# Performance work log

Hardware: AMD Instinct MI355X
Metric: run time of the kernel (lower is better)

Reference implementation:

```python
import jax, jax.numpy as jnp
import numpy as np

N = 50000       # num vertices
E_SEG = 80000   # num hyperedges
NNZ = 400000    # incidence pairs
FIN = 512       # input feature dim
H = 256         # MLP_hidden
C = 40          # num classes
NLAYER = 2      # All_num_layers
ALPHA = 0.5     # restart_alpha


def _w(k, shape):
    return jax.random.normal(k, shape, jnp.float32) * (1.0 / np.sqrt(shape[0]))


def setup_inputs() -> dict:
    key = jax.random.key(0)
    ks = jax.random.split(key, 12)
    return {
        "x": jax.random.normal(ks[0], (N, FIN), jnp.float32),
        "vertex": jax.random.randint(ks[1], (NNZ,), 0, N),
        "edges": jax.random.randint(ks[2], (NNZ,), 0, E_SEG),
        "lin_in_w": _w(ks[3], (FIN, H)), "lin_in_b": jnp.zeros((H,), jnp.float32),
        "w1": _w(ks[4], (H, H)),   "b1": jnp.zeros((H,), jnp.float32),
        "w2": _w(ks[5], (2 * H, H)), "b2": jnp.zeros((H,), jnp.float32),
        "w3": _w(ks[6], (H, H)),   "b3": jnp.zeros((H,), jnp.float32),
        "cls_w1": _w(ks[7], (H, H)), "cls_b1": jnp.zeros((H,), jnp.float32),
        "cls_w2": _w(ks[8], (H, C)), "cls_b2": jnp.zeros((C,), jnp.float32),
    }


def reference(x, vertex, edges, lin_in_w, lin_in_b, w1, b1, w2, b2, w3, b3,
              cls_w1, cls_b1, cls_w2, cls_b2):
    # input projection (dropout is identity at p=0)
    x = jax.nn.relu(x @ lin_in_w + lin_in_b)           # [N, H]
    x0 = x
    for _ in range(NLAYER):  # same conv weights reused each layer
        # W1 (1-layer MLP = Linear), gather to incidences
        xve = (x @ w1 + b1)[vertex]                    # [NNZ, H]
        # scatter-add to hyperedges
        xe = jax.ops.segment_sum(xve, edges, num_segments=E_SEG)  # [E, H]
        # gather back, concat with vertex feats, W2 (Linear on 2H)
        xev = jnp.concatenate([x[vertex], xe[edges]], axis=-1) @ w2 + b2  # [NNZ, H]
        # scatter-add to vertices
        xv = jax.ops.segment_sum(xev, vertex, num_segments=N)     # [N, H]
        # restart connection + W (Linear) + outer activation
        x = (1.0 - ALPHA) * xv + ALPHA * x0
        x = jax.nn.relu(x @ w3 + b3)
    # classifier MLP (2 layers: Linear -> relu -> Linear)
    h = jax.nn.relu(x @ cls_w1 + cls_b1)
    return h @ cls_w2 + cls_b2                          # [N, C]
```

## Files before the change

kernel.cpp:

```cpp
#include <hip/hip_runtime.h>
#include <hip/hip_bf16.h>
#include <cstdint>
#include <cstddef>

#define HD   256
#define NV   50000
#define NE   80000
#define NNZC 400000
#define FINC 512
#define NCLS 40

using bf16 = __hip_bfloat16;

typedef short bf16x8v __attribute__((ext_vector_type(8)));
typedef float f32x4   __attribute__((ext_vector_type(4)));
typedef unsigned short u16x8 __attribute__((ext_vector_type(8)));

#define NCH_E ((NE + 1023) / 1024)
#define NCH_V ((NV + 1023) / 1024)
#define NBM_V ((NV + 127) / 128)

__device__ __forceinline__ float b2f(unsigned short u) {
    union { unsigned int i; float f; } c; c.i = ((unsigned int)u) << 16; return c.f;
}
__device__ __forceinline__ unsigned short f2b(float f) {
    union { float f; unsigned int i; } c; c.f = f;
    return (unsigned short)((c.i + 0x7FFFu + ((c.i >> 16) & 1u)) >> 16);
}
__device__ __forceinline__ float4 load4f(const bf16* p) {
    ushort4 u = *reinterpret_cast<const ushort4*>(p);
    return make_float4(b2f(u.x), b2f(u.y), b2f(u.z), b2f(u.w));
}
__device__ __forceinline__ void store4(bf16* p, float4 v) {
    ushort4 u; u.x = f2b(v.x); u.y = f2b(v.y); u.z = f2b(v.z); u.w = f2b(v.w);
    *reinterpret_cast<ushort4*>(p) = u;
}

__device__ __forceinline__ void gl_lds16(const bf16* g, short* l) {
    __builtin_amdgcn_global_load_lds(
        (const __attribute__((address_space(1))) unsigned int*)g,
        (__attribute__((address_space(3))) unsigned int*)l,
        16, 0, 0);
}

__global__ __launch_bounds__(256)
void fill0_k(unsigned int* __restrict__ p, long long n)
{
    long long i = (long long)blockIdx.x * 256 + threadIdx.x;
    long long stride = (long long)gridDim.x * 256;
    for (; i < n; i += stride) p[i] = 0u;
}

__global__ __launch_bounds__(256)
void hist_k(const int* __restrict__ vertex, const int* __restrict__ edges,
            int* __restrict__ cnt_v, int* __restrict__ cnt_e, int nnz)
{
    int i = blockIdx.x * 256 + threadIdx.x;
    if (i < nnz) {
        atomicAdd(&cnt_v[vertex[i]], 1);
        atomicAdd(&cnt_e[edges[i]], 1);
    }
}

__global__ __launch_bounds__(256)
void scan_part2_k(const int* __restrict__ cnt_e, int* __restrict__ off_e, int* __restrict__ part_e,
                  const int* __restrict__ cnt_v, int* __restrict__ off_v, int* __restrict__ part_v)
{
    const int* cnt; int* off; int* part; int n;
    if (blockIdx.y == 0) { cnt = cnt_e; off = off_e; part = part_e; n = NE; }
    else                 { cnt = cnt_v; off = off_v; part = part_v; n = NV; }
    int base = blockIdx.x * 1024;
    if (base >= n) return;
    __shared__ int s[256];
    int idx = base + threadIdx.x * 4;
    int v[4], sum = 0;
    #pragma unroll
    for (int j = 0; j < 4; ++j) { v[j] = (idx + j < n) ? cnt[idx + j] : 0; sum += v[j]; }
    s[threadIdx.x] = sum;
    __syncthreads();
    #pragma unroll
    for (int d = 1; d < 256; d <<= 1) {
        int t = (threadIdx.x >= d) ? s[threadIdx.x - d] : 0;
        __syncthreads();
        s[threadIdx.x] += t;
        __syncthreads();
    }
    int excl = s[threadIdx.x] - sum;
    #pragma unroll
    for (int j = 0; j < 4; ++j) {
        if (idx + j < n) off[idx + j] = excl;
        excl += v[j];
    }
    if (threadIdx.x == 255) part[blockIdx.x] = s[255];
}

__global__ __launch_bounds__(256)
void scan_top2_k(int* __restrict__ part_e, int* __restrict__ end_e,
                 int* __restrict__ part_v, int* __restrict__ end_v)
{
    int* part; int* endp; int nch;
    if (blockIdx.x == 0) { part = part_e; endp = end_e; nch = NCH_E; }
    else                 { part = part_v; endp = end_v; nch = NCH_V; }
    __shared__ int s[256];
    int v = (threadIdx.x < nch) ? part[threadIdx.x] : 0;
    s[threadIdx.x] = v;
    __syncthreads();
    #pragma unroll
    for (int d = 1; d < 256; d <<= 1) {
        int t = (threadIdx.x >= d) ? s[threadIdx.x - d] : 0;
        __syncthreads();
        s[threadIdx.x] += t;
        __syncthreads();
    }
    if (threadIdx.x < nch) part[threadIdx.x] = s[threadIdx.x] - v;
    if (threadIdx.x == 255) *endp = s[255];
}

__global__ __launch_bounds__(256)
void scan_addcur2_k(int* __restrict__ off_e, const int* __restrict__ part_e, int* __restrict__ cur_e,
                    int* __restrict__ off_v, const int* __restrict__ part_v, int* __restrict__ cur_v)
{
    int n; int* off; const int* part; int* cur;
    if (blockIdx.y == 0) { n = NE; off = off_e; part = part_e; cur = cur_e; }
    else                 { n = NV; off = off_v; part = part_v; cur = cur_v; }
    int i = blockIdx.x * 256 + threadIdx.x;
    if (i < n) { int o = off[i] + part[i >> 10]; off[i] = o; cur[i] = o; }
}

__global__ __launch_bounds__(256)
void csr_fill_k(const int* __restrict__ vertex, const int* __restrict__ edges,
                int* __restrict__ cur_e, int* __restrict__ cur_v,
                int* __restrict__ adj_e, int* __restrict__ adj_v, int nnz)
{
    int i = blockIdx.x * 256 + threadIdx.x;
    if (i >= nnz) return;
    int v = vertex[i], e = edges[i];
    adj_e[atomicAdd(&cur_e[e], 1)] = v;
    adj_v[atomicAdd(&cur_v[v], 1)] = e;
}

__global__ __launch_bounds__(256)
void dege2_k(const int* __restrict__ cnt_e, const int* __restrict__ adj_v,
             const int* __restrict__ off_v, int* __restrict__ dege2, int n)
{
    int v = blockIdx.x * 256 + threadIdx.x;
    if (v >= n) return;
    int s = 0;
    for (int j = off_v[v]; j < off_v[v + 1]; ++j) s += cnt_e[adj_v[j]];
    dege2[v] = s;
}

__global__ __launch_bounds__(256)
void b1w23_k(const float* __restrict__ b1, const unsigned short* __restrict__ W23bt,
             float* __restrict__ o)
{
    int n = threadIdx.x;
    float s = 0.f;
    for (int k = 0; k < 256; ++k) s += b1[k] * b2f(W23bt[n * 256 + k]);
    o[n] = s;
}

__global__ __launch_bounds__(256)
void prep_w_k(const float* __restrict__ lin_w, const float* __restrict__ w1,
              const float* __restrict__ w2, const float* __restrict__ w3,
              const float* __restrict__ cw1, const float* __restrict__ cw2,
              const float* __restrict__ b2,
              unsigned short* __restrict__ lin_wt, unsigned short* __restrict__ w1_nb,
              unsigned short* __restrict__ w2a_nb, unsigned short* __restrict__ w2b_nb,
              unsigned short* __restrict__ w3t, unsigned short* __restrict__ cw1t,
              unsigned short* __restrict__ cw2t, float* __restrict__ b2w3)
{
    int idx = blockIdx.x * 256 + threadIdx.x;
    if (idx < 131072) { int n = idx >> 9, k = idx & 511; lin_wt[idx] = f2b(lin_w[k * 256 + n]); return; }
    idx -= 131072;
    if (idx < 65536) { w1_nb[idx] = f2b(w1[idx]); return; }
    idx -= 65536;
    if (idx < 65536) { w2a_nb[idx] = f2b(w2[idx]); return; }
    idx -= 65536;
    if (idx < 65536) { w2b_nb[idx] = f2b(w2[65536 + idx]); return; }
    idx -= 65536;
    if (idx < 65536) { int n = idx >> 8, k = idx & 255; w3t[idx] = f2b(w3[k * 256 + n]); return; }
    idx -= 65536;
    if (idx < 65536) { int n = idx >> 8, k = idx & 255; cw1t[idx] = f2b(cw1[k * 256 + n]); return; }
    idx -= 65536;
    if (idx < 12288) { int n = idx >> 8, k = idx & 255; cw2t[idx] = f2b((n < NCLS) ? cw2[k * NCLS + n] : 0.f); return; }
    idx -= 12288;
    if (idx < 256) {
        float s = 0.f;
        for (int k = 0; k < 256; ++k) s += b2[k] * w3[k * 256 + idx];
        b2w3[idx] = s;
    }
}

template<int EPI, bool AF32>
__global__ __launch_bounds__(256)
void mgemm_k(const void* __restrict__ Agv, const bf16* __restrict__ Bt,
             const float* __restrict__ bias, const float* __restrict__ bias2,
             const int* __restrict__ deg, const int* __restrict__ dege2,
             const bf16* __restrict__ Sb, const bf16* __restrict__ z0b,
             const float* __restrict__ b2w3v, const float* __restrict__ b1w23v,
             bf16* __restrict__ Cg, bf16* __restrict__ Cg2, bf16* __restrict__ Cg3,
             int M, int K, int Nc)
{
    const int nbn = Nc >> 7;
    const int nbm = (M + 127) >> 7;
    const int p   = blockIdx.x;
    const int xcd = p & 7;
    const int q   = p >> 3;
    const int cblk = q % nbn;
    const int rblk = q / nbn;
    const int rb   = rblk * 8 + xcd;
    if (rb >= nbm) return;
    const int bn = cblk * 128;
    const int bm = rb * 128;

    __shared__ __align__(16) short As[128 * 64];
    __shared__ __align__(16) short Bs[128 * 64];

    const int t  = threadIdx.x;
    const int wv = t >> 6, l = t & 63;
    const int wr = wv >> 1, wc = wv & 1;
    const int l15 = l & 15;

    f32x4 acc[4][4];
    #pragma unroll
    for (int m = 0; m < 4; ++m)
        #pragma unroll
        for (int n = 0; n < 4; ++n)
            acc[m][n] = (f32x4){0.f, 0.f, 0.f, 0.f};

    const int brow8   = l >> 3;
    const int bcol_sw = (((l & 7) ^ (l >> 3)) * 8);

    for (int k0 = 0; k0 < K; k0 += 64) {
        if constexpr (AF32) {
            const float* Af = (const float*)Agv;
            #pragma unroll
            for (int pi = 0; pi < 4; ++pi) {
                int idx8 = pi * 256 + t;
                int row  = idx8 >> 3;
                int cg   = (idx8 & 7) * 8;
                int ga = bm + row; if (ga >= M) ga = M - 1;
                const float* src = Af + (size_t)ga * K + k0 + cg;
                f32x4 u = *reinterpret_cast<const f32x4*>(src);
                f32x4 v = *reinterpret_cast<const f32x4*>(src + 4);
                bf16x8v o;
                o[0] = (short)f2b(u[0]); o[1] = (short)f2b(u[1]);
                o[2] = (short)f2b(u[2]); o[3] = (short)f2b(u[3]);
                o[4] = (short)f2b(v[0]); o[5] = (short)f2b(v[1]);
                o[6] = (short)f2b(v[2]); o[7] = (short)f2b(v[3]);
                *reinterpret_cast<bf16x8v*>(As + row * 64 + (cg ^ ((row & 7) * 8))) = o;
            }
        } else {
            const bf16* Ab = (const bf16*)Agv;
            #pragma unroll
            for (int i = 0; i < 4; ++i) {
                int c = wv * 4 + i;
                int row = c * 8 + brow8;
                int ga = bm + row; if (ga >= M) ga = M - 1;
                gl_lds16(Ab + (size_t)ga * K + k0 + bcol_sw, As + c * 512);
            }
        }
        #pragma unroll
        for (int i = 0; i < 4; ++i) {
            int c = wv * 4 + i;
            int row = c * 8 + brow8;
            gl_lds16(Bt + (size_t)(bn + row) * K + k0 + bcol_sw, Bs + c * 512);
        }
        __syncthreads();

        #pragma unroll
        for (int ks = 0; ks < 2; ++ks) {
            bf16x8v a[4], b[4];
            const int kb = ks * 64 + (l >> 4) * 16;
            #pragma unroll
            for (int m = 0; m < 4; ++m) {
                int r = wr * 64 + m * 16 + l15;
                a[m] = *reinterpret_cast<const bf16x8v*>(
                           (const char*)As + r * 128 + (kb ^ ((r & 7) << 4)));
            }
            #pragma unroll
            for (int n = 0; n < 4; ++n) {
                int r = wc * 64 + n * 16 + l15;
                b[n] = *reinterpret_cast<const bf16x8v*>(
                           (const char*)Bs + r * 128 + (kb ^ ((r & 7) << 4)));
            }
            #pragma unroll
            for (int m = 0; m < 4; ++m)
                #pragma unroll
                for (int n = 0; n < 4; ++n)
                    acc[m][n] = __builtin_amdgcn_mfma_f32_16x16x32_bf16(a[m], b[n], acc[m][n], 0, 0, 0);
        }
        __syncthreads();
    }

    if (EPI == 5) {
        int oi = bn >> 8;
        bf16* CC = (oi == 0) ? Cg : Cg2;
        int c2 = (bn >> 7) & 1;
        unsigned short* P = (unsigned short*)CC + ((size_t)(rb * 2 + c2) * 256 + t) * 64;
        #pragma unroll
        for (int m = 0; m < 4; ++m) {
            u16x8 o0, o1;
            #pragma unroll
            for (int n = 0; n < 2; ++n)
                #pragma unroll
                for (int i = 0; i < 4; ++i) {
                    o0[n * 4 + i] = f2b(acc[m][n][i]);
                    o1[n * 4 + i] = f2b(acc[m][n + 2][i]);
                }
            *reinterpret_cast<u16x8*>(P + m * 16)     = o0;
            *reinterpret_cast<u16x8*>(P + m * 16 + 8) = o1;
        }
    } else if (EPI == 4) {
        float bv[4], bw[4], bb1[4];
        #pragma unroll
        for (int n = 0; n < 4; ++n) {
            int col = bn + wc * 64 + n * 16 + l15;
            bv[n]  = bias[col];
            bw[n]  = b2w3v[col];
            bb1[n] = b1w23v[col];
        }
        const unsigned short* Sp = (const unsigned short*)Sb + ((size_t)(rb * 2 + cblk) * 256 + t) * 64;
        const unsigned short* Zp = (const unsigned short*)z0b + ((size_t)(rb * 2 + cblk) * 256 + t) * 64;
        u16x8 sv8[8], zv8[8];
        #pragma unroll
        for (int j = 0; j < 8; ++j) {
            sv8[j] = *reinterpret_cast<const u16x8*>(Sp + j * 8);
            zv8[j] = *reinterpret_cast<const u16x8*>(Zp + j * 8);
        }
        #pragma unroll
        for (int m = 0; m < 4; ++m) {
            #pragma unroll
            for (int i = 0; i < 4; ++i) {
                int row = bm + wr * 64 + m * 16 + (l >> 4) * 4 + i;
                if (row >= M) continue;
                float d   = (float)deg[row];
                float de2 = (float)dege2[row];
                size_t base = (size_t)row * Nc + bn + wc * 64 + l15;
                #pragma unroll
                for (int n = 0; n < 4; ++n) {
                    int e = m * 16 + n * 4 + i;
                    float sv = b2f(sv8[e >> 3][e & 7]);
                    float zv = b2f(zv8[e >> 3][e & 7]);
                    float v = 0.5f * (d * (sv + bw[n]) + acc[m][n][i] + de2 * bb1[n])
                              + 0.5f * zv + bv[n];
                    v = fmaxf(v, 0.f);
                    reinterpret_cast<unsigned short*>(Cg)[base + (size_t)n * 16] = f2b(v);
                }
            }
        }
    } else if (EPI == 3) {
        int oi = bn >> 8;
        bf16* CC = (oi == 0) ? Cg : (oi == 1) ? Cg2 : Cg3;
        const float* bb = (oi == 0) ? bias : (oi == 1) ? bias2 : nullptr;
        int cb = bn & 255;
        float bv[4];
        #pragma unroll
        for (int n = 0; n < 4; ++n)
            bv[n] = bb ? bb[cb + wc * 64 + n * 16 + l15] : 0.f;
        #pragma unroll
        for (int m = 0; m < 4; ++m) {
            #pragma unroll
            for (int i = 0; i < 4; ++i) {
                int row = bm + wr * 64 + m * 16 + (l >> 4) * 4 + i;
                if (row >= M) continue;
                size_t base = (size_t)row * 256 + cb + wc * 64 + l15;
                #pragma unroll
                for (int n = 0; n < 4; ++n)
                    reinterpret_cast<unsigned short*>(CC)[base + n * 16] = f2b(acc[m][n][i] + bv[n]);
            }
        }
    } else {
        float bv[4];
        #pragma unroll
        for (int n = 0; n < 4; ++n)
            bv[n] = bias ? bias[bn + wc * 64 + n * 16 + l15] : 0.f;
        #pragma unroll
        for (int m = 0; m < 4; ++m) {
            #pragma unroll
            for (int i = 0; i < 4; ++i) {
                int row = bm + wr * 64 + m * 16 + (l >> 4) * 4 + i;
                if (row >= M) continue;
                size_t base = (size_t)row * Nc + bn + wc * 64 + l15;
                #pragma unroll
                for (int n = 0; n < 4; ++n) {
                    float v = acc[m][n][i] + bv[n];
                    if (EPI == 1) v = fmaxf(v, 0.f);
                    reinterpret_cast<unsigned short*>(Cg)[base + n * 16] = f2b(v);
                }
            }
        }
    }
}

__global__ __launch_bounds__(256)
void gather_sum_k(const bf16* __restrict__ src, const int* __restrict__ adj,
                  const int* __restrict__ off, bf16* __restrict__ dst, int nseg)
{
    int seg = blockIdx.x * 4 + (threadIdx.x >> 6);
    if (seg >= nseg) return;
    int lane = threadIdx.x & 63;
    int s0 = off[seg], s1 = off[seg + 1];
    float4 acc = make_float4(0.f, 0.f, 0.f, 0.f);
    int j = s0;
    for (; j + 4 <= s1; j += 4) {
        int r0 = adj[j], r1 = adj[j + 1], r2 = adj[j + 2], r3 = adj[j + 3];
        float4 v0 = load4f(src + (size_t)r0 * HD + lane * 4);
        float4 v1 = load4f(src + (size_t)r1 * HD + lane * 4);
        float4 v2 = load4f(src + (size_t)r2 * HD + lane * 4);
        float4 v3 = load4f(src + (size_t)r3 * HD + lane * 4);
        acc.x += (v0.x + v1.x) + (v2.x + v3.x);
        acc.y += (v0.y + v1.y) + (v2.y + v3.y);
        acc.z += (v0.z + v1.z) + (v2.z + v3.z);
        acc.w += (v0.w + v1.w) + (v2.w + v3.w);
    }
    for (; j < s1; ++j) {
        float4 v = load4f(src + (size_t)adj[j] * HD + lane * 4);
        acc.x += v.x; acc.y += v.y; acc.z += v.z; acc.w += v.w;
    }
    store4(dst + (size_t)seg * HD + lane * 4, acc);
}

__global__ __launch_bounds__(256)
void cls_mfma_k(const bf16* __restrict__ Hm, const bf16* __restrict__ Wt,
                const float* __restrict__ bias, float* __restrict__ out, int M)
{
    const int wv = threadIdx.x >> 6, l = threadIdx.x & 63;
    const int l15 = l & 15;
    const int r0 = blockIdx.x * 64 + wv * 16;
    f32x4 acc[3];
    #pragma unroll
    for (int n = 0; n < 3; ++n) acc[n] = (f32x4){0.f, 0.f, 0.f, 0.f};

    int arow = r0 + l15; if (arow >= M) arow = M - 1;
    const int ko = (l >> 4) * 8;
    for (int kk = 0; kk < HD; kk += 32) {
        bf16x8v a = *reinterpret_cast<const bf16x8v*>(Hm + (size_t)arow * HD + kk + ko);
        #pragma unroll
        for (int n = 0; n < 3; ++n) {
            bf16x8v b = *reinterpret_cast<const bf16x8v*>(Wt + (size_t)(n * 16 + l15) * HD + kk + ko);
            acc[n] = __builtin_amdgcn_mfma_f32_16x16x32_bf16(a, b, acc[n], 0, 0, 0);
        }
    }
    #pragma unroll
    for (int n = 0; n < 3; ++n) {
        int col = n * 16 + l15;
        if (col >= NCLS) continue;
        float bv = bias[col];
        #pragma unroll
        for (int i = 0; i < 4; ++i) {
            int row = r0 + (l >> 4) * 4 + i;
            if (row < M) out[(size_t)row * NCLS + col] = acc[n][i] + bv;
        }
    }
}

static inline int xcd_grid(int M, int Nc)
{
    int nbm = (M + 127) >> 7;
    int nbn = Nc >> 7;
    return nbn * (((nbm + 7) / 8) * 8);
}

extern "C" void kernel_launch(void* const* d_in, const int* in_sizes, int n_in,
                              void* d_out, int out_size, void* d_ws, size_t ws_size,
                              hipStream_t stream)
{
    const float* x_in   = (const float*)d_in[0];
    const int*   vertex = (const int*)d_in[1];
    const int*   edges  = (const int*)d_in[2];
    const float* lin_w  = (const float*)d_in[3];
    const float* lin_b  = (const float*)d_in[4];
    const float* w1     = (const float*)d_in[5];
    const float* b1     = (const float*)d_in[6];
    const float* w2     = (const float*)d_in[7];
    const float* b2     = (const float*)d_in[8];
    const float* w3     = (const float*)d_in[9];
    const float* b3     = (const float*)d_in[10];
    const float* cw1    = (const float*)d_in[11];
    const float* cb1    = (const float*)d_in[12];
    const float* cw2    = (const float*)d_in[13];
    const float* cb2    = (const float*)d_in[14];
    float* out = (float*)d_out;
    (void)in_sizes; (void)n_in; (void)out_size; (void)ws_size;

    char* ws = (char*)d_ws;
    const size_t nvhd = (size_t)NV * HD, nehd = (size_t)NE * HD;
    const size_t permsz = (size_t)(NBM_V + 1) * 2 * 256 * 64;
    size_t off = 0;
    auto alloc = [&](size_t bytes) { char* p = ws + off; off += (bytes + 255) & ~(size_t)255; return p; };
    bf16* x0 = (bf16*)alloc(nvhd * 2);
    bf16* xA = (bf16*)alloc(nvhd * 2);
    bf16* E1 = (bf16*)alloc(nehd * 2);
    bf16* E2 = (bf16*)alloc(nehd * 2);
    bf16* S  = (bf16*)alloc(permsz * 2);
    bf16* z0 = (bf16*)alloc(permsz * 2);
    unsigned short* W23at  = (unsigned short*)alloc(2 * 256 * 256 * 2);
    unsigned short* w3t    = W23at + 65536;
    unsigned short* W23bt  = (unsigned short*)alloc(256 * 256 * 2);
    unsigned short* W123bt = (unsigned short*)alloc(256 * 256 * 2);
    unsigned short* w2ab   = (unsigned short*)alloc(512 * 256 * 2);
    unsigned short* w2a_nb = w2ab;
    unsigned short* w2b_nb = w2ab + 256 * 256;
    unsigned short* w1_nb  = (unsigned short*)alloc(256 * 256 * 2);
    unsigned short* lin_wt = (unsigned short*)alloc(256 * 512 * 2);
    unsigned short* cw1t   = (unsigned short*)alloc(256 * 256 * 2);
    unsigned short* cw2t   = (unsigned short*)alloc(48 * 256 * 2);
    float* b2w3  = (float*)alloc(256 * 4);
    float* b1w23 = (float*)alloc(256 * 4);
    int* cnt_e = (int*)alloc(NE * 4);
    int* cnt_v = (int*)alloc(NV * 4);
    int* dege2 = (int*)alloc(NV * 4);
    int* off_e = (int*)alloc((NE + 1) * 4);
    int* off_v = (int*)alloc((NV + 1) * 4);
    int* cur_e = (int*)alloc(NE * 4);
    int* cur_v = (int*)alloc(NV * 4);
    int* part_e = (int*)alloc(256 * 4);
    int* part_v = (int*)alloc(256 * 4);
    int* adj_e = (int*)alloc((size_t)NNZC * 4);
    int* adj_v = (int*)alloc((size_t)NNZC * 4);

    dim3 blk(256);

    fill0_k<<<128, blk, 0, stream>>>((unsigned int*)cnt_e, NE + NV);
    hist_k<<<(NNZC + 255) / 256, blk, 0, stream>>>(vertex, edges, cnt_v, cnt_e, NNZC);
    scan_part2_k<<<dim3(NCH_E, 2), blk, 0, stream>>>(cnt_e, off_e, part_e, cnt_v, off_v, part_v);
    scan_top2_k<<<2, blk, 0, stream>>>(part_e, off_e + NE, part_v, off_v + NV);
    scan_addcur2_k<<<dim3((NE + 255) / 256, 2), blk, 0, stream>>>(off_e, part_e, cur_e,
                                                                  off_v, part_v, cur_v);
    csr_fill_k<<<(NNZC + 255) / 256, blk, 0, stream>>>(vertex, edges, cur_e, cur_v, adj_e, adj_v, NNZC);
    dege2_k<<<(NV + 255) / 256, blk, 0, stream>>>(cnt_e, adj_v, off_v, dege2, NV);

    prep_w_k<<<1841, blk, 0, stream>>>(lin_w, w1, w2, w3, cw1, cw2, b2,
                                       lin_wt, w1_nb, w2a_nb, w2b_nb, w3t, cw1t, cw2t, b2w3);
    mgemm_k<3, false><<<xcd_grid(256, 512), blk, 0, stream>>>((const bf16*)w3t, (const bf16*)w2ab,
        nullptr, nullptr, nullptr, nullptr, nullptr, nullptr, nullptr, nullptr,
        (bf16*)W23at, (bf16*)W23bt, nullptr, 256, 256, 512);
    mgemm_k<0, false><<<xcd_grid(256, 256), blk, 0, stream>>>((const bf16*)W23bt, (const bf16*)w1_nb,
        nullptr, nullptr, nullptr, nullptr, nullptr, nullptr, nullptr, nullptr,
        (bf16*)W123bt, nullptr, nullptr, 256, 256, 256);
    b1w23_k<<<1, blk, 0, stream>>>(b1, W23bt, b1w23);

    mgemm_k<1, true><<<xcd_grid(NV, 256), blk, 0, stream>>>(x_in, (const bf16*)lin_wt,
        lin_b, nullptr, nullptr, nullptr, nullptr, nullptr, nullptr, nullptr,
        x0, nullptr, nullptr, NV, FINC, HD);

    const bf16* cur = x0;
    for (int layer = 0; layer < 2; ++layer) {
        if (layer == 0) {
            mgemm_k<5, false><<<xcd_grid(NV, 512), blk, 0, stream>>>(cur, (const bf16*)W23at,
                nullptr, nullptr, nullptr, nullptr, nullptr, nullptr, nullptr, nullptr,
                S, z0, nullptr, NV, HD, 512);
        } else {
            mgemm_k<5, false><<<xcd_grid(NV, 256), blk, 0, stream>>>(cur, (const bf16*)W23at,
                nullptr, nullptr, nullptr, nullptr, nullptr, nullptr, nullptr, nullptr,
                S, nullptr, nullptr, NV, HD, HD);
        }
        gather_sum_k<<<(NE + 3) / 4, blk, 0, stream>>>(cur, adj_e, off_e, E2, NE);
        gather_sum_k<<<(NV + 3) / 4, blk, 0, stream>>>(E2, adj_v, off_v, E1, NV);
        mgemm_k<4, false><<<xcd_grid(NV, 256), blk, 0, stream>>>(E1, (const bf16*)W123bt,
            b3, nullptr, cnt_v, dege2, S, z0, b2w3, b1w23,
            xA, nullptr, nullptr, NV, HD, HD);
        cur = xA;
    }

    mgemm_k<1, false><<<xcd_grid(NV, 256), blk, 0, stream>>>(xA, (const bf16*)cw1t,
        cb1, nullptr, nullptr, nullptr, nullptr, nullptr, nullptr, nullptr,
        E1, nullptr, nullptr, NV, HD, HD);
    cls_mfma_k<<<(NV + 63) / 64, blk, 0, stream>>>(E1, (const bf16*)cw2t, cb2, out, NV);
}
```

Before: 487.0 us.

## Co-schedule GEMM with edge gather in one launch and merge fill with weight prep

Merges the per-layer S/z0 GEMM and the hyperedge gather-sum into a single kernel that splits blocks by index, so the memory-bound gather runs alongside the MFMA GEMM blocks. The buffer-zeroing kernel is also folded into the weight-prep kernel to remove a launch. In the EPI==4 GEMM, the S/z0 and bias epilogue loads move before the main loop so their latency overlaps compute, at the cost of more live registers during the loop.

```diff
diff --git a/kernel.cpp b/kernel.cpp
--- a/kernel.cpp
+++ b/kernel.cpp
@@ -43,134 +43,50 @@
         16, 0, 0);
 }
 
-__global__ __launch_bounds__(256)
-void fill0_k(unsigned int* __restrict__ p, long long n)
-{
-    long long i = (long long)blockIdx.x * 256 + threadIdx.x;
-    long long stride = (long long)gridDim.x * 256;
-    for (; i < n; i += stride) p[i] = 0u;
-}
-
-__global__ __launch_bounds__(256)
-void hist_k(const int* __restrict__ vertex, const int* __restrict__ edges,
-            int* __restrict__ cnt_v, int* __restrict__ cnt_e, int nnz)
-{
-    int i = blockIdx.x * 256 + threadIdx.x;
-    if (i < nnz) {
-        atomicAdd(&cnt_v[vertex[i]], 1);
-        atomicAdd(&cnt_e[edges[i]], 1);
-    }
-}
-
-__global__ __launch_bounds__(256)
-void scan_part2_k(const int* __restrict__ cnt_e, int* __restrict__ off_e, int* __restrict__ part_e,
-                  const int* __restrict__ cnt_v, int* __restrict__ off_v, int* __restrict__ part_v)
-{
-    const int* cnt; int* off; int* part; int n;
-    if (blockIdx.y == 0) { cnt = cnt_e; off = off_e; part = part_e; n = NE; }
-    else                 { cnt = cnt_v; off = off_v; part = part_v; n = NV; }
-    int base = blockIdx.x * 1024;
-    if (base >= n) return;
-    __shared__ int s[256];
-    int idx = base + threadIdx.x * 4;
-    int v[4], sum = 0;
-    #pragma unroll
-    for (int j = 0; j < 4; ++j) { v[j] = (idx + j < n) ? cnt[idx + j] : 0; sum += v[j]; }
-    s[threadIdx.x] = sum;
-    __syncthreads();
-    #pragma unroll
-    for (int d = 1; d < 256; d <<= 1) {
-        int t = (threadIdx.x >= d) ? s[threadIdx.x - d] : 0;
-        __syncthreads();
-        s[threadIdx.x] += t;
-        __syncthreads();
-    }
-    int excl = s[threadIdx.x] - sum;
-    #pragma unroll
-    for (int j = 0; j < 4; ++j) {
-        if (idx + j < n) off[idx + j] = excl;
-        excl += v[j];
-    }
-    if (threadIdx.x == 255) part[blockIdx.x] = s[255];
-}
-
-__global__ __launch_bounds__(256)
-void scan_top2_k(int* __restrict__ part_e, int* __restrict__ end_e,
-                 int* __restrict__ part_v, int* __restrict__ end_v)
-{
-    int* part; int* endp; int nch;
-    if (blockIdx.x == 0) { part = part_e; endp = end_e; nch = NCH_E; }
-    else                 { part = part_v; endp = end_v; nch = NCH_V; }
-    __shared__ int s[256];
-    int v = (threadIdx.x < nch) ? part[threadIdx.x] : 0;
-    s[threadIdx.x] = v;
-    __syncthreads();
-    #pragma unroll
-    for (int d = 1; d < 256; d <<= 1) {
-        int t = (threadIdx.x >= d) ? s[threadIdx.x - d] : 0;
-        __syncthreads();
-        s[threadIdx.x] += t;
-        __syncthreads();
-    }
-    if (threadIdx.x < nch) part[threadIdx.x] = s[threadIdx.x] - v;
-    if (threadIdx.x == 255) *endp = s[255];
-}
-
-__global__ __launch_bounds__(256)
-void scan_addcur2_k(int* __restrict__ off_e, const int* __restrict__ part_e, int* __restrict__ cur_e,
-                    int* __restrict__ off_v, const int* __restrict__ part_v, int* __restrict__ cur_v)
-{
-    int n; int* off; const int* part; int* cur;
-    if (blockIdx.y == 0) { n = NE; off = off_e; part = part_e; cur = cur_e; }
-    else                 { n = NV; off = off_v; part = part_v; cur = cur_v; }
-    int i = blockIdx.x * 256 + threadIdx.x;
-    if (i < n) { int o = off[i] + part[i >> 10]; off[i] = o; cur[i] = o; }
-}
-
-__global__ __launch_bounds__(256)
-void csr_fill_k(const int* __restrict__ vertex, const int* __restrict__ edges,
-                int* __restrict__ cur_e, int* __restrict__ cur_v,
-                int* __restrict__ adj_e, int* __restrict__ adj_v, int nnz)
-{
-    int i = blockIdx.x * 256 + threadIdx.x;
-    if (i >= nnz) return;
-    int v = vertex[i], e = edges[i];
-    adj_e[atomicAdd(&cur_e[e], 1)] = v;
-    adj_v[atomicAdd(&cur_v[v], 1)] = e;
-}
-
-__global__ __launch_bounds__(256)
-void dege2_k(const int* __restrict__ cnt_e, const int* __restrict__ adj_v,
-             const int* __restrict__ off_v, int* __restrict__ dege2, int n)
-{
-    int v = blockIdx.x * 256 + threadIdx.x;
-    if (v >= n) return;
-    int s = 0;
-    for (int j = off_v[v]; j < off_v[v + 1]; ++j) s += cnt_e[adj_v[j]];
-    dege2[v] = s;
-}
-
-__global__ __launch_bounds__(256)
-void b1w23_k(const float* __restrict__ b1, const unsigned short* __restrict__ W23bt,
-             float* __restrict__ o)
-{
-    int n = threadIdx.x;
-    float s = 0.f;
-    for (int k = 0; k < 256; ++k) s += b1[k] * b2f(W23bt[n * 256 + k]);
-    o[n] = s;
-}
-
-__global__ __launch_bounds__(256)
-void prep_w_k(const float* __restrict__ lin_w, const float* __restrict__ w1,
-              const float* __restrict__ w2, const float* __restrict__ w3,
-              const float* __restrict__ cw1, const float* __restrict__ cw2,
-              const float* __restrict__ b2,
-              unsigned short* __restrict__ lin_wt, unsigned short* __restrict__ w1_nb,
-              unsigned short* __restrict__ w2a_nb, unsigned short* __restrict__ w2b_nb,
-              unsigned short* __restrict__ w3t, unsigned short* __restrict__ cw1t,
-              unsigned short* __restrict__ cw2t, float* __restrict__ b2w3)
-{
-    int idx = blockIdx.x * 256 + threadIdx.x;
+__device__ __forceinline__ void gather_body(const bf16* __restrict__ src,
+                                            const int* __restrict__ adj,
+                                            const int* __restrict__ off,
+                                            bf16* __restrict__ dst,
+                                            int seg, int lane)
+{
+    int s0 = off[seg], s1 = off[seg + 1];
+    float4 acc = make_float4(0.f, 0.f, 0.f, 0.f);
+    int j = s0;
+    for (; j + 4 <= s1; j += 4) {
+        int r0 = adj[j], r1 = adj[j + 1], r2 = adj[j + 2], r3 = adj[j + 3];
+        float4 v0 = load4f(src + (size_t)r0 * HD + lane * 4);
+        float4 v1 = load4f(src + (size_t)r1 * HD + lane * 4);
+        float4 v2 = load4f(src + (size_t)r2 * HD + lane * 4);
+        float4 v3 = load4f(src + (size_t)r3 * HD + lane * 4);
+        acc.x += (v0.x + v1.x) + (v2.x + v3.x);
+        acc.y += (v0.y + v1.y) + (v2.y + v3.y);
+        acc.z += (v0.z + v1.z) + (v2.z + v3.z);
+        acc.w += (v0.w + v1.w) + (v2.w + v3.w);
+    }
+    for (; j < s1; ++j) {
+        float4 v = load4f(src + (size_t)adj[j] * HD + lane * 4);
+        acc.x += v.x; acc.y += v.y; acc.z += v.z; acc.w += v.w;
+    }
+    store4(dst + (size_t)seg * HD + lane * 4, acc);
+}
+
+__global__ __launch_bounds__(256)
+void fill_prep_k(unsigned int* __restrict__ fillp, long long filln,
+                 const float* __restrict__ lin_w, const float* __restrict__ w1,
+                 const float* __restrict__ w2, const float* __restrict__ w3,
+                 const float* __restrict__ cw1, const float* __restrict__ cw2,
+                 const float* __restrict__ b2,
+                 unsigned short* __restrict__ lin_wt, unsigned short* __restrict__ w1_nb,
+                 unsigned short* __restrict__ w2a_nb, unsigned short* __restrict__ w2b_nb,
+                 unsigned short* __restrict__ w3t, unsigned short* __restrict__ cw1t,
+                 unsigned short* __restrict__ cw2t, float* __restrict__ b2w3)
+{
+    if (blockIdx.x < 128) {
+        long long i = (long long)blockIdx.x * 256 + threadIdx.x;
+        for (; i < filln; i += 128 * 256) fillp[i] = 0u;
+        return;
+    }
+    int idx = (blockIdx.x - 128) * 256 + threadIdx.x;
     if (idx < 131072) { int n = idx >> 9, k = idx & 511; lin_wt[idx] = f2b(lin_w[k * 256 + n]); return; }
     idx -= 131072;
     if (idx < 65536) { w1_nb[idx] = f2b(w1[idx]); return; }
@@ -192,6 +108,115 @@
     }
 }
 
+__global__ __launch_bounds__(256)
+void hist_k(const int* __restrict__ vertex, const int* __restrict__ edges,
+            int* __restrict__ cnt_v, int* __restrict__ cnt_e, int nnz)
+{
+    int i = blockIdx.x * 256 + threadIdx.x;
+    if (i < nnz) {
+        atomicAdd(&cnt_v[vertex[i]], 1);
+        atomicAdd(&cnt_e[edges[i]], 1);
+    }
+}
+
+__global__ __launch_bounds__(256)
+void scan_part2_k(const int* __restrict__ cnt_e, int* __restrict__ off_e, int* __restrict__ part_e,
+                  const int* __restrict__ cnt_v, int* __restrict__ off_v, int* __restrict__ part_v)
+{
+    const int* cnt; int* off; int* part; int n;
+    if (blockIdx.y == 0) { cnt = cnt_e; off = off_e; part = part_e; n = NE; }
+    else                 { cnt = cnt_v; off = off_v; part = part_v; n = NV; }
+    int base = blockIdx.x * 1024;
+    if (base >= n) return;
+    __shared__ int s[256];
+    int idx = base + threadIdx.x * 4;
+    int v[4], sum = 0;
+    #pragma unroll
+    for (int j = 0; j < 4; ++j) { v[j] = (idx + j < n) ? cnt[idx + j] : 0; sum += v[j]; }
+    s[threadIdx.x] = sum;
+    __syncthreads();
+    #pragma unroll
+    for (int d = 1; d < 256; d <<= 1) {
+        int t = (threadIdx.x >= d) ? s[threadIdx.x - d] : 0;
+        __syncthreads();
+        s[threadIdx.x] += t;
+        __syncthreads();
+    }
+    int excl = s[threadIdx.x] - sum;
+    #pragma unroll
+    for (int j = 0; j < 4; ++j) {
+        if (idx + j < n) off[idx + j] = excl;
+        excl += v[j];
+    }
+    if (threadIdx.x == 255) part[blockIdx.x] = s[255];
+}
+
+__global__ __launch_bounds__(256)
+void scan_top2_k(int* __restrict__ part_e, int* __restrict__ end_e,
+                 int* __restrict__ part_v, int* __restrict__ end_v)
+{
+    int* part; int* endp; int nch;
+    if (blockIdx.x == 0) { part = part_e; endp = end_e; nch = NCH_E; }
+    else                 { part = part_v; endp = end_v; nch = NCH_V; }
+    __shared__ int s[256];
+    int v = (threadIdx.x < nch) ? part[threadIdx.x] : 0;
+    s[threadIdx.x] = v;
+    __syncthreads();
+    #pragma unroll
+    for (int d = 1; d < 256; d <<= 1) {
+        int t = (threadIdx.x >= d) ? s[threadIdx.x - d] : 0;
+        __syncthreads();
+        s[threadIdx.x] += t;
+        __syncthreads();
+    }
+    if (threadIdx.x < nch) part[threadIdx.x] = s[threadIdx.x] - v;
+    if (threadIdx.x == 255) *endp = s[255];
+}
+
+__global__ __launch_bounds__(256)
+void scan_addcur2_k(int* __restrict__ off_e, const int* __restrict__ part_e, int* __restrict__ cur_e,
+                    int* __restrict__ off_v, const int* __restrict__ part_v, int* __restrict__ cur_v)
+{
+    int n; int* off; const int* part; int* cur;
+    if (blockIdx.y == 0) { n = NE; off = off_e; part = part_e; cur = cur_e; }
+    else                 { n = NV; off = off_v; part = part_v; cur = cur_v; }
+    int i = blockIdx.x * 256 + threadIdx.x;
+    if (i < n) { int o = off[i] + part[i >> 10]; off[i] = o; cur[i] = o; }
+}
+
+__global__ __launch_bounds__(256)
+void csr_fill_k(const int* __restrict__ vertex, const int* __restrict__ edges,
+                int* __restrict__ cur_e, int* __restrict__ cur_v,
+                int* __restrict__ adj_e, int* __restrict__ adj_v, int nnz)
+{
+    int i = blockIdx.x * 256 + threadIdx.x;
+    if (i >= nnz) return;
+    int v = vertex[i], e = edges[i];
+    adj_e[atomicAdd(&cur_e[e], 1)] = v;
+    adj_v[atomicAdd(&cur_v[v], 1)] = e;
+}
+
+__global__ __launch_bounds__(256)
+void dege2_k(const int* __restrict__ cnt_e, const int* __restrict__ adj_v,
+             const int* __restrict__ off_v, int* __restrict__ dege2, int n)
+{
+    int v = blockIdx.x * 256 + threadIdx.x;
+    if (v >= n) return;
+    int s = 0;
+    for (int j = off_v[v]; j < off_v[v + 1]; ++j) s += cnt_e[adj_v[j]];
+    dege2[v] = s;
+}
+
+__global__ __launch_bounds__(256)
+void b1w23_k(const float* __restrict__ b1, const unsigned short* __restrict__ W23bt,
+             float* __restrict__ o)
+{
+    int n = threadIdx.x;
+    float s = 0.f;
+    for (int k = 0; k < 256; ++k) s += b1[k] * b2f(W23bt[n * 256 + k]);
+    o[n] = s;
+}
+
 template<int EPI, bool AF32>
 __global__ __launch_bounds__(256)
 void mgemm_k(const void* __restrict__ Agv, const bf16* __restrict__ Bt,
@@ -221,6 +246,25 @@
     const int wv = t >> 6, l = t & 63;
     const int wr = wv >> 1, wc = wv & 1;
     const int l15 = l & 15;
+
+    u16x8 sv8[8], zv8[8];
+    float bv[4], bw[4], bb1[4];
+    if (EPI == 4) {
+        const unsigned short* Sp = (const unsigned short*)Sb + ((size_t)(rb * 2 + cblk) * 256 + t) * 64;
+        const unsigned short* Zp = (const unsigned short*)z0b + ((size_t)(rb * 2 + cblk) * 256 + t) * 64;
+        #pragma unroll
+        for (int j = 0; j < 8; ++j) {
+            sv8[j] = *reinterpret_cast<const u16x8*>(Sp + j * 8);
+            zv8[j] = *reinterpret_cast<const u16x8*>(Zp + j * 8);
+        }
+        #pragma unroll
+        for (int n = 0; n < 4; ++n) {
+            int col = bn + wc * 64 + n * 16 + l15;
+            bv[n]  = bias[col];
+            bw[n]  = b2w3v[col];
+            bb1[n] = b1w23v[col];
+        }
+    }
 
     f32x4 acc[4][4];
     #pragma unroll
@@ -313,22 +357,6 @@
             *reinterpret_cast<u16x8*>(P + m * 16 + 8) = o1;
         }
     } else if (EPI == 4) {
-        float bv[4], bw[4], bb1[4];
-        #pragma unroll
-        for (int n = 0; n < 4; ++n) {
-            int col = bn + wc * 64 + n * 16 + l15;
-            bv[n]  = bias[col];
-            bw[n]  = b2w3v[col];
-            bb1[n] = b1w23v[col];
-        }
-        const unsigned short* Sp = (const unsigned short*)Sb + ((size_t)(rb * 2 + cblk) * 256 + t) * 64;
-        const unsigned short* Zp = (const unsigned short*)z0b + ((size_t)(rb * 2 + cblk) * 256 + t) * 64;
-        u16x8 sv8[8], zv8[8];
-        #pragma unroll
-        for (int j = 0; j < 8; ++j) {
-            sv8[j] = *reinterpret_cast<const u16x8*>(Sp + j * 8);
-            zv8[j] = *reinterpret_cast<const u16x8*>(Zp + j * 8);
-        }
         #pragma unroll
         for (int m = 0; m < 4; ++m) {
             #pragma unroll
@@ -355,10 +383,10 @@
         bf16* CC = (oi == 0) ? Cg : (oi == 1) ? Cg2 : Cg3;
         const float* bb = (oi == 0) ? bias : (oi == 1) ? bias2 : nullptr;
         int cb = bn & 255;
-        float bv[4];
+        float bvv[4];
         #pragma unroll
         for (int n = 0; n < 4; ++n)
-            bv[n] = bb ? bb[cb + wc * 64 + n * 16 + l15] : 0.f;
+            bvv[n] = bb ? bb[cb + wc * 64 + n * 16 + l15] : 0.f;
         #pragma unroll
         for (int m = 0; m < 4; ++m) {
             #pragma unroll
@@ -368,14 +396,14 @@
                 size_t base = (size_t)row * 256 + cb + wc * 64 + l15;
                 #pragma unroll
                 for (int n = 0; n < 4; ++n)
-                    reinterpret_cast<unsigned short*>(CC)[base + n * 16] = f2b(acc[m][n][i] + bv[n]);
+                    reinterpret_cast<unsigned short*>(CC)[base + n * 16] = f2b(acc[m][n][i] + bvv[n]);
             }
         }
     } else {
-        float bv[4];
+        float bvv[4];
         #pragma unroll
         for (int n = 0; n < 4; ++n)
-            bv[n] = bias ? bias[bn + wc * 64 + n * 16 + l15] : 0.f;
+            bvv[n] = bias ? bias[bn + wc * 64 + n * 16 + l15] : 0.f;
         #pragma unroll
         for (int m = 0; m < 4; ++m) {
             #pragma unroll
@@ -385,7 +413,7 @@
                 size_t base = (size_t)row * Nc + bn + wc * 64 + l15;
                 #pragma unroll
                 for (int n = 0; n < 4; ++n) {
-                    float v = acc[m][n][i] + bv[n];
+                    float v = acc[m][n][i] + bvv[n];
                     if (EPI == 1) v = fmaxf(v, 0.f);
                     reinterpret_cast<unsigned short*>(Cg)[base + n * 16] = f2b(v);
                 }
@@ -395,31 +423,115 @@
 }
 
 __global__ __launch_bounds__(256)
+void fusedA_k(const bf16* __restrict__ Ag, const bf16* __restrict__ Bt,
+              bf16* __restrict__ Sg, bf16* __restrict__ z0g,
+              int M, int K, int Nc, int gemmBlocks,
+              const bf16* __restrict__ gsrc, const int* __restrict__ adj,
+              const int* __restrict__ off, bf16* __restrict__ gdst, int nseg)
+{
+    __shared__ __align__(16) short As[128 * 64];
+    __shared__ __align__(16) short Bs[128 * 64];
+    const int t = threadIdx.x;
+
+    if ((int)blockIdx.x >= gemmBlocks) {
+        int seg = (blockIdx.x - gemmBlocks) * 4 + (t >> 6);
+        if (seg < nseg) gather_body(gsrc, adj, off, gdst, seg, t & 63);
+        return;
+    }
+
+    const int nbn = Nc >> 7;
+    const int nbm = (M + 127) >> 7;
+    const int p   = blockIdx.x;
+    const int xcd = p & 7;
+    const int q   = p >> 3;
+    const int cblk = q % nbn;
+    const int rblk = q / nbn;
+    const int rb   = rblk * 8 + xcd;
+    if (rb >= nbm) return;
+    const int bn = cblk * 128;
+    const int bm = rb * 128;
+
+    const int wv = t >> 6, l = t & 63;
+    const int wr = wv >> 1, wc = wv & 1;
+    const int l15 = l & 15;
+
+    f32x4 acc[4][4];
+    #pragma unroll
+    for (int m = 0; m < 4; ++m)
+        #pragma unroll
+        for (int n = 0; n < 4; ++n)
+            acc[m][n] = (f32x4){0.f, 0.f, 0.f, 0.f};
+
+    const int brow8   = l >> 3;
+    const int bcol_sw = (((l & 7) ^ (l >> 3)) * 8);
+
+    for (int k0 = 0; k0 < K; k0 += 64) {
+        #pragma unroll
+        for (int i = 0; i < 4; ++i) {
+            int c = wv * 4 + i;
+            int row = c * 8 + brow8;
+            int ga = bm + row; if (ga >= M) ga = M - 1;
+            gl_lds16(Ag + (size_t)ga * K + k0 + bcol_sw, As + c * 512);
+        }
+        #pragma unroll
+        for (int i = 0; i < 4; ++i) {
+            int c = wv * 4 + i;
+            int row = c * 8 + brow8;
+            gl_lds16(Bt + (size_t)(bn + row) * K + k0 + bcol_sw, Bs + c * 512);
+        }
+        __syncthreads();
+
+        #pragma unroll
+        for (int ks = 0; ks < 2; ++ks) {
+            bf16x8v a[4], b[4];
+            const int kb = ks * 64 + (l >> 4) * 16;
+            #pragma unroll
+            for (int m = 0; m < 4; ++m) {
+                int r = wr * 64 + m * 16 + l15;
+                a[m] = *reinterpret_cast<const bf16x8v*>(
+                           (const char*)As + r * 128 + (kb ^ ((r & 7) << 4)));
+            }
+            #pragma unroll
+            for (int n = 0; n < 4; ++n) {
+                int r = wc * 64 + n * 16 + l15;
+                b[n] = *reinterpret_cast<const bf16x8v*>(
+                           (const char*)Bs + r * 128 + (kb ^ ((r & 7) << 4)));
+            }
+            #pragma unroll
+            for (int m = 0; m < 4; ++m)
+                #pragma unroll
+                for (int n = 0; n < 4; ++n)
+                    acc[m][n] = __builtin_amdgcn_mfma_f32_16x16x32_bf16(a[m], b[n], acc[m][n], 0, 0, 0);
+        }
+        __syncthreads();
+    }
+
+    int oi = bn >> 8;
+    bf16* CC = (oi == 0) ? Sg : z0g;
+    int c2 = (bn >> 7) & 1;
+    unsigned short* P = (unsigned short*)CC + ((size_t)(rb * 2 + c2) * 256 + t) * 64;
+    #pragma unroll
+    for (int m = 0; m < 4; ++m) {
+        u16x8 o0, o1;
+        #pragma unroll
+        for (int n = 0; n < 2; ++n)
+            #pragma unroll
+            for (int i = 0; i < 4; ++i) {
+                o0[n * 4 + i] = f2b(acc[m][n][i]);
+                o1[n * 4 + i] = f2b(acc[m][n + 2][i]);
+            }
+        *reinterpret_cast<u16x8*>(P + m * 16)     = o0;
+        *reinterpret_cast<u16x8*>(P + m * 16 + 8) = o1;
+    }
+}
+
+__global__ __launch_bounds__(256)
 void gather_sum_k(const bf16* __restrict__ src, const int* __restrict__ adj,
                   const int* __restrict__ off, bf16* __restrict__ dst, int nseg)
 {
     int seg = blockIdx.x * 4 + (threadIdx.x >> 6);
     if (seg >= nseg) return;
-    int lane = threadIdx.x & 63;
-    int s0 = off[seg], s1 = off[seg + 1];
-    float4 acc = make_float4(0.f, 0.f, 0.f, 0.f);
-    int j = s0;
-    for (; j + 4 <= s1; j += 4) {
-        int r0 = adj[j], r1 = adj[j + 1], r2 = adj[j + 2], r3 = adj[j + 3];
-        float4 v0 = load4f(src + (size_t)r0 * HD + lane * 4);
-        float4 v1 = load4f(src + (size_t)r1 * HD + lane * 4);
-        float4 v2 = load4f(src + (size_t)r2 * HD + lane * 4);
-        float4 v3 = load4f(src + (size_t)r3 * HD + lane * 4);
-        acc.x += (v0.x + v1.x) + (v2.x + v3.x);
-        acc.y += (v0.y + v1.y) + (v2.y + v3.y);
-        acc.z += (v0.z + v1.z) + (v2.z + v3.z);
-        acc.w += (v0.w + v1.w) + (v2.w + v3.w);
-    }
-    for (; j < s1; ++j) {
-        float4 v = load4f(src + (size_t)adj[j] * HD + lane * 4);
-        acc.x += v.x; acc.y += v.y; acc.z += v.z; acc.w += v.w;
-    }
-    store4(dst + (size_t)seg * HD + lane * 4, acc);
+    gather_body(src, adj, off, dst, seg, threadIdx.x & 63);
 }
 
 __global__ __launch_bounds__(256)
@@ -522,8 +634,11 @@
     int* adj_v = (int*)alloc((size_t)NNZC * 4);
 
     dim3 blk(256);
-
-    fill0_k<<<128, blk, 0, stream>>>((unsigned int*)cnt_e, NE + NV);
+    const int gatherE_blocks = (NE + 3) / 4;
+
+    fill_prep_k<<<128 + 1841, blk, 0, stream>>>((unsigned int*)cnt_e, NE + NV,
+        lin_w, w1, w2, w3, cw1, cw2, b2,
+        lin_wt, w1_nb, w2a_nb, w2b_nb, w3t, cw1t, cw2t, b2w3);
     hist_k<<<(NNZC + 255) / 256, blk, 0, stream>>>(vertex, edges, cnt_v, cnt_e, NNZC);
     scan_part2_k<<<dim3(NCH_E, 2), blk, 0, stream>>>(cnt_e, off_e, part_e, cnt_v, off_v, part_v);
     scan_top2_k<<<2, blk, 0, stream>>>(part_e, off_e + NE, part_v, off_v + NV);
@@ -532,8 +647,6 @@
     csr_fill_k<<<(NNZC + 255) / 256, blk, 0, stream>>>(vertex, edges, cur_e, cur_v, adj_e, adj_v, NNZC);
     dege2_k<<<(NV + 255) / 256, blk, 0, stream>>>(cnt_e, adj_v, off_v, dege2, NV);
 
-    prep_w_k<<<1841, blk, 0, stream>>>(lin_w, w1, w2, w3, cw1, cw2, b2,
-                                       lin_wt, w1_nb, w2a_nb, w2b_nb, w3t, cw1t, cw2t, b2w3);
     mgemm_k<3, false><<<xcd_grid(256, 512), blk, 0, stream>>>((const bf16*)w3t, (const bf16*)w2ab,
         nullptr, nullptr, nullptr, nullptr, nullptr, nullptr, nullptr, nullptr,
         (bf16*)W23at, (bf16*)W23bt, nullptr, 256, 256, 512);
@@ -548,16 +661,10 @@
 
     const bf16* cur = x0;
     for (int layer = 0; layer < 2; ++layer) {
-        if (layer == 0) {
-            mgemm_k<5, false><<<xcd_grid(NV, 512), blk, 0, stream>>>(cur, (const bf16*)W23at,
-                nullptr, nullptr, nullptr, nullptr, nullptr, nullptr, nullptr, nullptr,
-                S, z0, nullptr, NV, HD, 512);
-        } else {
-            mgemm_k<5, false><<<xcd_grid(NV, 256), blk, 0, stream>>>(cur, (const bf16*)W23at,
-                nullptr, nullptr, nullptr, nullptr, nullptr, nullptr, nullptr, nullptr,
-                S, nullptr, nullptr, NV, HD, HD);
-        }
-        gather_sum_k<<<(NE + 3) / 4, blk, 0, stream>>>(cur, adj_e, off_e, E2, NE);
+        int Nc_s = (layer == 0) ? 512 : 256;
+        int gb = xcd_grid(NV, Nc_s);
+        fusedA_k<<<gb + gatherE_blocks, blk, 0, stream>>>(cur, (const bf16*)W23at,
+            S, z0, NV, HD, Nc_s, gb, cur, adj_e, off_e, E2, NE);
         gather_sum_k<<<(NV + 3) / 4, blk, 0, stream>>>(E2, adj_v, off_v, E1, NV);
         mgemm_k<4, false><<<xcd_grid(NV, 256), blk, 0, stream>>>(E1, (const bf16*)W123bt,
             b3, nullptr, cnt_v, dege2, S, z0, b2w3, b1w23,
```

New measurement: 535.0 us. 1.1x slower.
